# Kernel optimization log

Hardware: AMD Instinct MI355X
Metric: run time of the kernel (lower is better)

## Reference

```python
import jax, jax.numpy as jnp
import numpy as np

B, T, F = 64, 8192, 6
MODES, WIDTH, LAYERS = 32, 64, 4
FC1, OUT = 128, 7


def setup_inputs() -> dict:
    key = jax.random.key(0)
    ks = jax.random.split(key, 8)
    def glorot(k, shape, fan_in, fan_out):
        return jax.random.normal(k, shape, jnp.float32) * np.float32(np.sqrt(2.0 / (fan_in + fan_out)))
    inputs = jax.random.normal(ks[0], (B, T, F), jnp.float32)
    fc0_w = glorot(ks[1], (F, WIDTH), F, WIDTH)
    fc0_b = jnp.zeros((WIDTH,), jnp.float32)
    fourier_wr = glorot(ks[2], (LAYERS, MODES, WIDTH, WIDTH), WIDTH, WIDTH)
    fourier_wi = glorot(ks[3], (LAYERS, MODES, WIDTH, WIDTH), WIDTH, WIDTH)
    conv_w = glorot(ks[4], (LAYERS, WIDTH, WIDTH), WIDTH, WIDTH)
    conv_b = jnp.zeros((LAYERS, WIDTH), jnp.float32)
    fc1_w = glorot(ks[5], (WIDTH, FC1), WIDTH, FC1)
    fc1_b = jnp.zeros((FC1,), jnp.float32)
    fc2_w = glorot(ks[6], (FC1, OUT), FC1, OUT)
    fc2_b = jnp.zeros((OUT,), jnp.float32)
    return {"inputs": inputs, "fc0_w": fc0_w, "fc0_b": fc0_b,
            "fourier_wr": fourier_wr, "fourier_wi": fourier_wi,
            "conv_w": conv_w, "conv_b": conv_b,
            "fc1_w": fc1_w, "fc1_b": fc1_b, "fc2_w": fc2_w, "fc2_b": fc2_b}


def _fourier_layer_time(x, wr, wi):
    # x: [B, T, C]; wr/wi: [MODES, C, C]
    t = x.shape[1]
    x_ft = jnp.fft.rfft(x, axis=1)              # [B, T//2+1, C] complex64
    tfreq = x_ft.shape[1]
    m = min(MODES, tfreq)
    w = (wr[:m] + 1j * wi[:m]).astype(jnp.complex64)   # [m, C, C]
    out_ft = jnp.einsum('bmc,mco->bmo', x_ft[:, :m, :], w)  # [B, m, C]
    out_ft = jnp.pad(out_ft, ((0, 0), (0, tfreq - m), (0, 0)))  # zero high modes
    return jnp.fft.irfft(out_ft, n=t, axis=1)   # [B, T, C] float32


def reference(inputs, fc0_w, fc0_b, fourier_wr, fourier_wi, conv_w, conv_b,
              fc1_w, fc1_b, fc2_w, fc2_b):
    x = inputs @ fc0_w + fc0_b                  # [B, T, WIDTH]
    for i in range(LAYERS):
        xf = _fourier_layer_time(x, fourier_wr[i], fourier_wi[i])
        x = jax.nn.gelu(xf + x @ conv_w[i] + conv_b[i], approximate=False)
    x = jax.nn.gelu(x @ fc1_w + fc1_b, approximate=False)   # [B, T, 128]
    out = x @ fc2_w + fc2_b                     # [B, T, 7]
    out = out.reshape(B, T, OUT, 1)
    return out[:, -1, :, :]                     # [B, 7, 1]
```

## Files before the change

kernel.cpp:

```cpp
#include <hip/hip_runtime.h>
#include <math.h>


constexpr int B = 64, T = 8192, F = 6, MODES = 32, C = 64, FC1N = 128, OUTN = 7;
constexpr int TMASK = T - 1;
constexpr int GCHF = 8;
constexpr int GCHC = 4;
constexpr int OSTR = 68;

typedef __attribute__((ext_vector_type(4))) float f32x4;
typedef __attribute__((ext_vector_type(8))) short s16x8;
typedef const __attribute__((address_space(1))) unsigned* gas_ptr;
typedef __attribute__((address_space(3))) unsigned* las_ptr;

__device__ __forceinline__ float gelu_exact(float v) {
    return 0.5f * v * (1.0f + erff(v * 0.70710678118654752f));
}
__device__ __forceinline__ float gelu_fast(float v) {
    float z = fabsf(v) * 0.70710678118654752f;
    float t = __builtin_amdgcn_rcpf(fmaf(0.3275911f, z, 1.0f));
    float p = fmaf(t, 1.061405429f, -1.453152027f);
    p = fmaf(t, p, 1.421413741f);
    p = fmaf(t, p, -0.284496736f);
    p = fmaf(t, p, 0.254829592f);
    p = p * t;
    float e = __expf(-z * z);
    float erfv = copysignf(fmaf(-p, e, 1.0f), v);
    return 0.5f * v * (1.0f + erfv);
}
__device__ __forceinline__ unsigned short bf16_rne(float f) {
    unsigned u = __float_as_uint(f);
    unsigned r = u + 0x7FFFu + ((u >> 16) & 1u);
    return (unsigned short)(r >> 16);
}
__device__ __forceinline__ float bf16_f(unsigned short h) {
    return __uint_as_float(((unsigned)h) << 16);
}
__device__ __forceinline__ unsigned pack_split(float v) {
    unsigned short hi = bf16_rne(v);
    float lo = v - bf16_f(hi);
    return (((unsigned)hi) << 16) | (unsigned)bf16_rne(lo);
}
__device__ __forceinline__ s16x8 u4_to_s8(uint4 v) {
    union { uint4 u; s16x8 s; } cv; cv.u = v; return cv.s;
}
__device__ __forceinline__ s16x8 hi8(uint4 p0, uint4 p1) {
    uint4 h;
    h.x = __byte_perm(p0.x, p0.y, 0x7632); h.y = __byte_perm(p0.z, p0.w, 0x7632);
    h.z = __byte_perm(p1.x, p1.y, 0x7632); h.w = __byte_perm(p1.z, p1.w, 0x7632);
    return u4_to_s8(h);
}
__device__ __forceinline__ s16x8 lo8(uint4 p0, uint4 p1) {
    uint4 h;
    h.x = __byte_perm(p0.x, p0.y, 0x5410); h.y = __byte_perm(p0.z, p0.w, 0x5410);
    h.z = __byte_perm(p1.x, p1.y, 0x5410); h.w = __byte_perm(p1.z, p1.w, 0x5410);
    return u4_to_s8(h);
}

__global__ void twdtab_k(unsigned short* __restrict__ twdH, unsigned short* __restrict__ twdL) {
    int i = blockIdx.x * 256 + threadIdx.x;
    int t = i >> 6, j = i & 63, k = j & 31;
    int m = (k * t) & TMASK;
    double th = 6.283185307179586476925286766559 * (double)m / (double)T;
    float v = (float)((j < 32) ? cos(th) : sin(th));
    unsigned short hi = bf16_rne(v);
    twdH[i] = hi;
    twdL[i] = bf16_rne(v - bf16_f(hi));
}

__global__ void twdtabT_k(unsigned* __restrict__ twdTP) {
    int i = blockIdx.x * 256 + threadIdx.x;
    int j = i >> 13, t = i & TMASK, k = j & 31;
    int m = (k * t) & TMASK;
    double th = 6.283185307179586476925286766559 * (double)m / (double)T;
    float v = (float)((j < 32) ? cos(th) : sin(th));
    twdTP[i] = pack_split(v);
}

__global__ void __launch_bounds__(256) fc0dft_k(const float* __restrict__ in,
                                                const float* __restrict__ w,
                                                const float* __restrict__ bias,
                                                const unsigned* __restrict__ twdTP,
                                                unsigned* __restrict__ x,
                                                float* __restrict__ partF) {
    __shared__ unsigned outT[64 * OSTR];
    int b = blockIdx.y, tid = threadIdx.x;
    int wv = tid >> 6, lane = tid & 63;
    int l15 = lane & 15, quad = lane >> 4;
    size_t bT = (size_t)b * T;

    int rr = tid & 15, cg = (tid >> 4) * 4;
    float wl[F][4], bl[4];
#pragma unroll
    for (int f = 0; f < F; f++)
#pragma unroll
        for (int j = 0; j < 4; j++) wl[f][j] = w[f * C + cg + j];
#pragma unroll
    for (int j = 0; j < 4; j++) bl[j] = bias[cg + j];

    const unsigned* atp = twdTP + (size_t)(wv * 16 + l15) * T;
    f32x4 dftacc[4];
#pragma unroll
    for (int nt = 0; nt < 4; nt++) dftacc[nt] = (f32x4){0.f, 0.f, 0.f, 0.f};

    int t0 = blockIdx.x * (64 * GCHF);
    for (int g = 0; g < GCHF; g++) {
        int tb = t0 + g * 64;
#pragma unroll
        for (int i = 0; i < 4; i++) {
            int r = rr + i * 16;
            int trow = tb + r;
            const float* ip = in + ((size_t)b * T + trow) * F;
            float i0 = ip[0], i1 = ip[1], i2 = ip[2], i3 = ip[3], i4 = ip[4], i5 = ip[5];
            uint4 pk;
            unsigned pv[4];
#pragma unroll
            for (int j = 0; j < 4; j++) {
                float v = bl[j];
                v = fmaf(i0, wl[0][j], v); v = fmaf(i1, wl[1][j], v);
                v = fmaf(i2, wl[2][j], v); v = fmaf(i3, wl[3][j], v);
                v = fmaf(i4, wl[4][j], v); v = fmaf(i5, wl[5][j], v);
                pv[j] = pack_split(v);
            }
            pk.x = pv[0]; pk.y = pv[1]; pk.z = pv[2]; pk.w = pv[3];
            *(uint4*)(x + (bT + trow) * C + cg) = pk;
            outT[(cg + 0) * OSTR + r] = pv[0];
            outT[(cg + 1) * OSTR + r] = pv[1];
            outT[(cg + 2) * OSTR + r] = pv[2];
            outT[(cg + 3) * OSTR + r] = pv[3];
        }
        __syncthreads();
#pragma unroll
        for (int ks = 0; ks < 2; ks++) {
            const unsigned* ap = atp + tb + ks * 32 + quad * 8;
            uint4 a0 = *(const uint4*)ap;
            uint4 a1 = *(const uint4*)(ap + 4);
            s16x8 ah = hi8(a0, a1), al = lo8(a0, a1);
#pragma unroll
            for (int nt = 0; nt < 4; nt++) {
                const unsigned* bp = &outT[(nt * 16 + l15) * OSTR + ks * 32 + quad * 8];
                uint4 b0 = *(const uint4*)bp;
                uint4 b1 = *(const uint4*)(bp + 4);
                s16x8 bh = hi8(b0, b1), bl2 = lo8(b0, b1);
                dftacc[nt] = __builtin_amdgcn_mfma_f32_16x16x32_bf16(ah, bh, dftacc[nt], 0, 0, 0);
                dftacc[nt] = __builtin_amdgcn_mfma_f32_16x16x32_bf16(ah, bl2, dftacc[nt], 0, 0, 0);
                dftacc[nt] = __builtin_amdgcn_mfma_f32_16x16x32_bf16(al, bh, dftacc[nt], 0, 0, 0);
            }
        }
        __syncthreads();
    }
    float sgn = (wv >= 2) ? -1.f : 1.f;
#pragma unroll
    for (int nt = 0; nt < 4; nt++)
#pragma unroll
        for (int r = 0; r < 4; r++) {
            int j = wv * 16 + quad * 4 + r;
            unsafeAtomicAdd(&partF[((size_t)b * 64 + j) * 64 + nt * 16 + l15],
                            sgn * dftacc[nt][r]);
        }
}

__global__ void mode_mix(const float* __restrict__ partF, const float* __restrict__ wr,
                         const float* __restrict__ wi, float2* __restrict__ Y) {
    int b = blockIdx.y, k = blockIdx.x, o = threadIdx.x;
    __shared__ float xr[C], xi[C];
    xr[o] = partF[((size_t)b * 64 + k) * 64 + o];
    xi[o] = partF[((size_t)b * 64 + 32 + k) * 64 + o];
    __syncthreads();
    float ar = 0.f, ai = 0.f;
    for (int c = 0; c < C; c++) {
        float wrr = wr[((size_t)k * C + c) * C + o];
        float wii = wi[((size_t)k * C + c) * C + o];
        float Xr = xr[c], Xi = xi[c];
        ar = fmaf(Xr, wrr, ar); ar = fmaf(-Xi, wii, ar);
        ai = fmaf(Xr, wii, ai); ai = fmaf(Xi, wrr, ai);
    }
    Y[((size_t)b * MODES + k) * C + o] = make_float2(ar, ai);
}

__global__ void bweights_k(const float2* __restrict__ Y, const float* __restrict__ cw,
                           unsigned short* __restrict__ Bw) {
    int b = blockIdx.x, tid = threadIdx.x;
    const float invT = 1.0f / (float)T;
    for (int i = tid; i < C * 256; i += 256) {
        int o = i >> 8, kc = i & 255;
        int src = kc & 127, half = kc >> 7;
        float w;
        if (src < 32) {
            float s = (src == 0) ? invT : 2.0f * invT;
            w = s * Y[((size_t)b * MODES + src) * C + o].x;
        } else if (src < 64) {
            w = (-2.0f * invT) * Y[((size_t)b * MODES + (src - 32)) * C + o].y;
        } else {
            w = cw[(size_t)(src - 64) * C + o];
        }
        unsigned short hi = bf16_rne(w);
        Bw[((size_t)b * C + o) * 256 + kc] = half ? bf16_rne(w - bf16_f(hi)) : hi;
    }
}

__global__ void __launch_bounds__(256) combine_mfma(unsigned* __restrict__ xp,
                                                    const unsigned short* __restrict__ twdH,
                                                    const unsigned short* __restrict__ twdL,
                                                    const unsigned* __restrict__ twdTP,
                                                    const unsigned short* __restrict__ Bw,
                                                    const float* __restrict__ cb,
                                                    float* __restrict__ partF) {
    __shared__ unsigned xs[2][4096];
    int b = blockIdx.y;
    int tid = threadIdx.x;
    int wv = tid >> 6, lane = tid & 63;
    int lm = lane & 15, quad = lane >> 4;
    int ncol = wv * 16 + lm;
    size_t bT = (size_t)b * T;
    int sA = (lm & 7) * 4;

    const unsigned short* bwp = Bw + ((size_t)b * C + ncol) * 256 + quad * 8;
    s16x8 bf0 = *(const s16x8*)(bwp + 0);
    s16x8 bf1 = *(const s16x8*)(bwp + 32);
    s16x8 bf2 = *(const s16x8*)(bwp + 64);
    s16x8 bf3 = *(const s16x8*)(bwp + 96);
    s16x8 bf4 = *(const s16x8*)(bwp + 128);
    s16x8 bf5 = *(const s16x8*)(bwp + 160);
    s16x8 bf6 = *(const s16x8*)(bwp + 192);
    s16x8 bf7 = *(const s16x8*)(bwp + 224);
    float cbv = cb[ncol];

    const unsigned* atp = twdTP + (size_t)(wv * 16 + lm) * T;
    f32x4 dftacc[4];
#pragma unroll
    for (int nt = 0; nt < 4; nt++) dftacc[nt] = (f32x4){0.f, 0.f, 0.f, 0.f};

    int g0 = blockIdx.x * GCHC;
    const unsigned* cbase = xp + (bT + (size_t)g0 * 64) * C;

    int soff[4];
#pragma unroll
    for (int p = 0; p < 4; p++) {
        int L = tid * 4 + p * 1024;
        int r = L >> 6, cl = L & 63;
        soff[p] = r * 64 + (cl ^ ((r & 7) * 4));
    }
#pragma unroll
    for (int p = 0; p < 4; p++)
        __builtin_amdgcn_global_load_lds((gas_ptr)(cbase + soff[p]),
                                         (las_ptr)(&xs[0][tid * 4 + p * 1024]), 16, 0, 0);

    for (int g = 0; g < GCHC; g++) {
        int t0 = (g0 + g) * 64;
        asm volatile("s_waitcnt vmcnt(0)" ::: "memory");
        __syncthreads();
        if (g + 1 < GCHC) {
            const unsigned* nbase = cbase + (size_t)(g + 1) * 4096;
#pragma unroll
            for (int p = 0; p < 4; p++)
                __builtin_amdgcn_global_load_lds((gas_ptr)(nbase + soff[p]),
                                                 (las_ptr)(&xs[(g + 1) & 1][tid * 4 + p * 1024]),
                                                 16, 0, 0);
        }
        unsigned* buf = xs[g & 1];
        f32x4 acc[4];
#pragma unroll
        for (int mt = 0; mt < 4; mt++) acc[mt] = (f32x4){0.f, 0.f, 0.f, 0.f};

#pragma unroll
        for (int mt = 0; mt < 4; mt++) {
            int rr = mt * 16 + lm;
            int t = t0 + rr;
            const unsigned short* thp = twdH + (size_t)t * C + quad * 8;
            const unsigned short* tlp = twdL + (size_t)t * C + quad * 8;
            const unsigned* xrp = buf + rr * 64;
            int base0 = (quad * 8) ^ sA;
            s16x8 a;
            a = *(const s16x8*)thp;
            acc[mt] = __builtin_amdgcn_mfma_f32_16x16x32_bf16(a, bf0, acc[mt], 0, 0, 0);
            acc[mt] = __builtin_amdgcn_mfma_f32_16x16x32_bf16(a, bf4, acc[mt], 0, 0, 0);
            a = *(const s16x8*)(thp + 32);
            acc[mt] = __builtin_amdgcn_mfma_f32_16x16x32_bf16(a, bf1, acc[mt], 0, 0, 0);
            acc[mt] = __builtin_amdgcn_mfma_f32_16x16x32_bf16(a, bf5, acc[mt], 0, 0, 0);
            uint4 p0 = *(const uint4*)(xrp + base0);
            uint4 p1 = *(const uint4*)(xrp + (base0 ^ 4));
            a = hi8(p0, p1);
            acc[mt] = __builtin_amdgcn_mfma_f32_16x16x32_bf16(a, bf2, acc[mt], 0, 0, 0);
            acc[mt] = __builtin_amdgcn_mfma_f32_16x16x32_bf16(a, bf6, acc[mt], 0, 0, 0);
            uint4 p2 = *(const uint4*)(xrp + (base0 ^ 32));
            uint4 p3 = *(const uint4*)(xrp + (base0 ^ 36));
            a = hi8(p2, p3);
            acc[mt] = __builtin_amdgcn_mfma_f32_16x16x32_bf16(a, bf3, acc[mt], 0, 0, 0);
            acc[mt] = __builtin_amdgcn_mfma_f32_16x16x32_bf16(a, bf7, acc[mt], 0, 0, 0);
            a = *(const s16x8*)tlp;
            acc[mt] = __builtin_amdgcn_mfma_f32_16x16x32_bf16(a, bf0, acc[mt], 0, 0, 0);
            a = *(const s16x8*)(tlp + 32);
            acc[mt] = __builtin_amdgcn_mfma_f32_16x16x32_bf16(a, bf1, acc[mt], 0, 0, 0);
            a = lo8(p0, p1);
            acc[mt] = __builtin_amdgcn_mfma_f32_16x16x32_bf16(a, bf2, acc[mt], 0, 0, 0);
            a = lo8(p2, p3);
            acc[mt] = __builtin_amdgcn_mfma_f32_16x16x32_bf16(a, bf3, acc[mt], 0, 0, 0);
        }
        __syncthreads();
#pragma unroll
        for (int mt = 0; mt < 4; mt++) {
            uint4 pk;
            unsigned pv[4];
#pragma unroll
            for (int r = 0; r < 4; r++) {
                int t = t0 + mt * 16 + quad * 4 + r;
                float v = acc[mt][r] + cbv;
                pv[r] = pack_split(gelu_fast(v));
                xp[(bT + t) * C + ncol] = pv[r];
            }
            pk.x = pv[0]; pk.y = pv[1]; pk.z = pv[2]; pk.w = pv[3];
            *(uint4*)(&buf[ncol * 64 + ((mt * 16 + quad * 4) ^ sA)]) = pk;
        }
        __syncthreads();
#pragma unroll
        for (int ks = 0; ks < 2; ks++) {
            const unsigned* ap = atp + t0 + ks * 32 + quad * 8;
            uint4 a0 = *(const uint4*)ap;
            uint4 a1 = *(const uint4*)(ap + 4);
            s16x8 ah = hi8(a0, a1), al = lo8(a0, a1);
#pragma unroll
            for (int nt = 0; nt < 4; nt++) {
                int cd = nt * 16 + lm;
                const unsigned* bpb = buf + cd * 64;
                int tb0 = (ks * 32 + quad * 8) ^ sA;
                uint4 b0 = *(const uint4*)(bpb + tb0);
                uint4 b1 = *(const uint4*)(bpb + (tb0 ^ 4));
                s16x8 bh = hi8(b0, b1), bl2 = lo8(b0, b1);
                dftacc[nt] = __builtin_amdgcn_mfma_f32_16x16x32_bf16(ah, bh, dftacc[nt], 0, 0, 0);
                dftacc[nt] = __builtin_amdgcn_mfma_f32_16x16x32_bf16(ah, bl2, dftacc[nt], 0, 0, 0);
                dftacc[nt] = __builtin_amdgcn_mfma_f32_16x16x32_bf16(al, bh, dftacc[nt], 0, 0, 0);
            }
        }
    }
    float sgn = (wv >= 2) ? -1.f : 1.f;
#pragma unroll
    for (int nt = 0; nt < 4; nt++)
#pragma unroll
        for (int r = 0; r < 4; r++) {
            int j = wv * 16 + quad * 4 + r;
            unsafeAtomicAdd(&partF[((size_t)b * 64 + j) * 64 + nt * 16 + lm],
                            sgn * dftacc[nt][r]);
        }
}

__global__ void final_k(const unsigned* __restrict__ x3, const float2* __restrict__ Y3,
                        const float* __restrict__ cw, const float* __restrict__ cb,
                        const float* __restrict__ w1, const float* __restrict__ b1,
                        const float* __restrict__ w2, const float* __restrict__ b2,
                        float* __restrict__ out) {
    int b = blockIdx.x, tid = threadIdx.x;
    __shared__ float xrow[C];
    __shared__ float xl[C];
    __shared__ float h[FC1N];
    if (tid < C) {
        unsigned u = x3[((size_t)b * T + (T - 1)) * C + tid];
        xrow[tid] = __uint_as_float(u & 0xFFFF0000u) + __uint_as_float(u << 16);
    }
    __syncthreads();
    if (tid < C) {
        int o = tid;
        const float2* Yb = Y3 + (size_t)b * (MODES * C);
        float a2 = 0.f;
        for (int k = 1; k < MODES; k++) {
            float thk = 7.6699039394282067e-4f * (float)k;
            float cwv = cosf(thk), swv = -sinf(thk);
            float2 y = Yb[k * C + o];
            a2 = fmaf(y.x, cwv, a2);
            a2 = fmaf(-y.y, swv, a2);
        }
        float xf = (Yb[o].x + 2.f * a2) * (1.0f / (float)T);
        float cv = cb[o];
        for (int c = 0; c < C; c++) cv = fmaf(xrow[c], cw[c * C + o], cv);
        xl[o] = gelu_exact(xf + cv);
    }
    __syncthreads();
    {
        int j = tid;
        float acc = b1[j];
        for (int c = 0; c < C; c++) acc = fmaf(xl[c], w1[c * FC1N + j], acc);
        h[j] = gelu_exact(acc);
    }
    __syncthreads();
    if (tid < OUTN) {
        float acc = b2[tid];
        for (int j = 0; j < FC1N; j++) acc = fmaf(h[j], w2[j * OUTN + tid], acc);
        out[b * OUTN + tid] = acc;
    }
}

extern "C" void kernel_launch(void* const* d_in, const int* in_sizes, int n_in,
                              void* d_out, int out_size, void* d_ws, size_t ws_size,
                              hipStream_t stream) {
    const float* inp   = (const float*)d_in[0];
    const float* fc0_w = (const float*)d_in[1];
    const float* fc0_b = (const float*)d_in[2];
    const float* fwr   = (const float*)d_in[3];
    const float* fwi   = (const float*)d_in[4];
    const float* cw    = (const float*)d_in[5];
    const float* cb    = (const float*)d_in[6];
    const float* w1    = (const float*)d_in[7];
    const float* b1    = (const float*)d_in[8];
    const float* w2    = (const float*)d_in[9];
    const float* b2    = (const float*)d_in[10];
    float* out = (float*)d_out;

    char* ws = (char*)d_ws;
    unsigned* x = (unsigned*)ws;
    size_t off = (size_t)B * T * C * sizeof(unsigned);
    float* partF = (float*)(ws + off);
    const size_t PART_BYTES = (size_t)B * 64 * 64 * sizeof(float);
    off += PART_BYTES;
    float2* Y = (float2*)(ws + off);
    off += (size_t)B * MODES * C * sizeof(float2);
    unsigned short* twdH = (unsigned short*)(ws + off);
    off += (size_t)T * C * sizeof(unsigned short);
    unsigned short* twdL = (unsigned short*)(ws + off);
    off += (size_t)T * C * sizeof(unsigned short);
    unsigned* twdTP = (unsigned*)(ws + off);
    off += (size_t)64 * T * sizeof(unsigned);
    unsigned short* Bw = (unsigned short*)(ws + off);
    off += (size_t)B * C * 256 * sizeof(unsigned short);

    twdtab_k<<<(T * C) / 256, 256, 0, stream>>>(twdH, twdL);
    twdtabT_k<<<(64 * T) / 256, 256, 0, stream>>>(twdTP);

    hipMemsetAsync(partF, 0, PART_BYTES, stream);
    fc0dft_k<<<dim3(T / (64 * GCHF), B), 256, 0, stream>>>(inp, fc0_w, fc0_b, twdTP, x, partF);

    for (int l = 0; l < 4; l++) {
        mode_mix<<<dim3(MODES, B), 64, 0, stream>>>(partF, fwr + (size_t)l * MODES * C * C,
                                                    fwi + (size_t)l * MODES * C * C, Y);
        if (l < 3) {
            hipMemsetAsync(partF, 0, PART_BYTES, stream);
            bweights_k<<<B, 256, 0, stream>>>(Y, cw + (size_t)l * C * C, Bw);
            combine_mfma<<<dim3(T / (64 * GCHC), B), 256, 0, stream>>>(x, twdH, twdL, twdTP, Bw,
                                                                       cb + (size_t)l * C, partF);
        }
    }
    final_k<<<B, FC1N, 0, stream>>>(x, Y, cw + (size_t)3 * C * C, cb + (size_t)3 * C,
                                    w1, b1, w2, b2, out);
}
```

Baseline: 553.8 us.

## Split twiddle tables into hi/lo planes, fuse mode-mix with weight build, retime prefetch

The transposed twiddle table is stored as separate bf16 hi and lo arrays, so the DFT A-fragments can be loaded directly instead of being unpacked with byte permutes. These loads are hoisted to the start of each chunk, and the fc0 input rows are read as float2 vectors. The mode_mix and bweights kernels are fused into one kernel with 256-thread blocks, removing a launch and a round trip of Y through memory. In combine_mfma, __syncthreads is replaced with hand-written waitcnt/barrier asm and the next-chunk LDS prefetch is issued later, after the first compute phase. The hand-tuned vmcnt count is a correctness risk if the compiler schedules loads differently than assumed.

After: 525.9 us. -5.0%, faster.

```diff
diff --git a/kernel.cpp b/kernel.cpp
--- a/kernel.cpp
+++ b/kernel.cpp
@@ -68,19 +68,22 @@
     twdL[i] = bf16_rne(v - bf16_f(hi));
 }
 
-__global__ void twdtabT_k(unsigned* __restrict__ twdTP) {
+__global__ void twdtabT_k(unsigned short* __restrict__ twdTPH, unsigned short* __restrict__ twdTPL) {
     int i = blockIdx.x * 256 + threadIdx.x;
     int j = i >> 13, t = i & TMASK, k = j & 31;
     int m = (k * t) & TMASK;
     double th = 6.283185307179586476925286766559 * (double)m / (double)T;
     float v = (float)((j < 32) ? cos(th) : sin(th));
-    twdTP[i] = pack_split(v);
+    unsigned short hi = bf16_rne(v);
+    twdTPH[i] = hi;
+    twdTPL[i] = bf16_rne(v - bf16_f(hi));
 }
 
 __global__ void __launch_bounds__(256) fc0dft_k(const float* __restrict__ in,
                                                 const float* __restrict__ w,
                                                 const float* __restrict__ bias,
-                                                const unsigned* __restrict__ twdTP,
+                                                const unsigned short* __restrict__ twdTPH,
+                                                const unsigned short* __restrict__ twdTPL,
                                                 unsigned* __restrict__ x,
                                                 float* __restrict__ partF) {
     __shared__ unsigned outT[64 * OSTR];
@@ -98,7 +101,8 @@
 #pragma unroll
     for (int j = 0; j < 4; j++) bl[j] = bias[cg + j];
 
-    const unsigned* atp = twdTP + (size_t)(wv * 16 + l15) * T;
+    const unsigned short* atpH = twdTPH + (size_t)(wv * 16 + l15) * T;
+    const unsigned short* atpL = twdTPL + (size_t)(wv * 16 + l15) * T;
     f32x4 dftacc[4];
 #pragma unroll
     for (int nt = 0; nt < 4; nt++) dftacc[nt] = (f32x4){0.f, 0.f, 0.f, 0.f};
@@ -106,12 +110,22 @@
     int t0 = blockIdx.x * (64 * GCHF);
     for (int g = 0; g < GCHF; g++) {
         int tb = t0 + g * 64;
+        float2 rin[4][3];
+#pragma unroll
+        for (int i = 0; i < 4; i++) {
+            const float2* ip2 = (const float2*)(in + ((size_t)b * T + tb + rr + i * 16) * F);
+            rin[i][0] = ip2[0]; rin[i][1] = ip2[1]; rin[i][2] = ip2[2];
+        }
+        s16x8 dAh0 = *(const s16x8*)(atpH + tb + quad * 8);
+        s16x8 dAl0 = *(const s16x8*)(atpL + tb + quad * 8);
+        s16x8 dAh1 = *(const s16x8*)(atpH + tb + 32 + quad * 8);
+        s16x8 dAl1 = *(const s16x8*)(atpL + tb + 32 + quad * 8);
 #pragma unroll
         for (int i = 0; i < 4; i++) {
             int r = rr + i * 16;
             int trow = tb + r;
-            const float* ip = in + ((size_t)b * T + trow) * F;
-            float i0 = ip[0], i1 = ip[1], i2 = ip[2], i3 = ip[3], i4 = ip[4], i5 = ip[5];
+            float i0 = rin[i][0].x, i1 = rin[i][0].y, i2 = rin[i][1].x;
+            float i3 = rin[i][1].y, i4 = rin[i][2].x, i5 = rin[i][2].y;
             uint4 pk;
             unsigned pv[4];
 #pragma unroll
@@ -129,13 +143,11 @@
             outT[(cg + 2) * OSTR + r] = pv[2];
             outT[(cg + 3) * OSTR + r] = pv[3];
         }
-        __syncthreads();
+        asm volatile("s_waitcnt lgkmcnt(0)\n\ts_barrier" ::: "memory");
 #pragma unroll
         for (int ks = 0; ks < 2; ks++) {
-            const unsigned* ap = atp + tb + ks * 32 + quad * 8;
-            uint4 a0 = *(const uint4*)ap;
-            uint4 a1 = *(const uint4*)(ap + 4);
-            s16x8 ah = hi8(a0, a1), al = lo8(a0, a1);
+            s16x8 ah = ks ? dAh1 : dAh0;
+            s16x8 al = ks ? dAl1 : dAl0;
 #pragma unroll
             for (int nt = 0; nt < 4; nt++) {
                 const unsigned* bp = &outT[(nt * 16 + l15) * OSTR + ks * 32 + quad * 8];
@@ -147,7 +159,7 @@
                 dftacc[nt] = __builtin_amdgcn_mfma_f32_16x16x32_bf16(al, bh, dftacc[nt], 0, 0, 0);
             }
         }
-        __syncthreads();
+        asm volatile("s_waitcnt lgkmcnt(0)\n\ts_barrier" ::: "memory");
     }
     float sgn = (wv >= 2) ? -1.f : 1.f;
 #pragma unroll
@@ -160,49 +172,64 @@
         }
 }
 
-__global__ void mode_mix(const float* __restrict__ partF, const float* __restrict__ wr,
-                         const float* __restrict__ wi, float2* __restrict__ Y) {
-    int b = blockIdx.y, k = blockIdx.x, o = threadIdx.x;
-    __shared__ float xr[C], xi[C];
-    xr[o] = partF[((size_t)b * 64 + k) * 64 + o];
-    xi[o] = partF[((size_t)b * 64 + 32 + k) * 64 + o];
+__global__ void __launch_bounds__(256) mixbw_k(const float* __restrict__ partF,
+                                               const float* __restrict__ wr,
+                                               const float* __restrict__ wi,
+                                               const float* __restrict__ cw,
+                                               float2* __restrict__ Y,
+                                               unsigned short* __restrict__ Bw,
+                                               int writeBw) {
+    __shared__ float xr[32][64], xi[32][64];
+    int b = blockIdx.x, q = blockIdx.y, tid = threadIdx.x;
+    int o = tid & 63, ks = tid >> 6;
+    const float* pb = partF + (size_t)b * 4096;
+    for (int i = tid; i < 2048; i += 256) xr[i >> 6][i & 63] = pb[i];
+    for (int i = tid; i < 2048; i += 256) xi[i >> 6][i & 63] = pb[2048 + i];
     __syncthreads();
-    float ar = 0.f, ai = 0.f;
-    for (int c = 0; c < C; c++) {
-        float wrr = wr[((size_t)k * C + c) * C + o];
-        float wii = wi[((size_t)k * C + c) * C + o];
-        float Xr = xr[c], Xi = xi[c];
-        ar = fmaf(Xr, wrr, ar); ar = fmaf(-Xi, wii, ar);
-        ai = fmaf(Xr, wii, ai); ai = fmaf(Xi, wrr, ai);
-    }
-    Y[((size_t)b * MODES + k) * C + o] = make_float2(ar, ai);
-}
-
-__global__ void bweights_k(const float2* __restrict__ Y, const float* __restrict__ cw,
-                           unsigned short* __restrict__ Bw) {
-    int b = blockIdx.x, tid = threadIdx.x;
     const float invT = 1.0f / (float)T;
-    for (int i = tid; i < C * 256; i += 256) {
-        int o = i >> 8, kc = i & 255;
-        int src = kc & 127, half = kc >> 7;
-        float w;
-        if (src < 32) {
-            float s = (src == 0) ? invT : 2.0f * invT;
-            w = s * Y[((size_t)b * MODES + src) * C + o].x;
-        } else if (src < 64) {
-            w = (-2.0f * invT) * Y[((size_t)b * MODES + (src - 32)) * C + o].y;
-        } else {
-            w = cw[(size_t)(src - 64) * C + o];
-        }
-        unsigned short hi = bf16_rne(w);
-        Bw[((size_t)b * C + o) * 256 + kc] = half ? bf16_rne(w - bf16_f(hi)) : hi;
+#pragma unroll
+    for (int s = 0; s < 2; s++) {
+        int k = q * 8 + ks * 2 + s;
+        float ar = 0.f, ai = 0.f;
+        const float* wrk = wr + (size_t)k * 4096 + o;
+        const float* wik = wi + (size_t)k * 4096 + o;
+        for (int c = 0; c < 64; c++) {
+            float wrr = wrk[(size_t)c * 64];
+            float wii = wik[(size_t)c * 64];
+            float Xr = xr[k][c], Xi = xi[k][c];
+            ar = fmaf(Xr, wrr, ar); ar = fmaf(-Xi, wii, ar);
+            ai = fmaf(Xr, wii, ai); ai = fmaf(Xi, wrr, ai);
+        }
+        Y[((size_t)b * MODES + k) * C + o] = make_float2(ar, ai);
+        if (writeBw) {
+            size_t base = ((size_t)b * C + o) * 256;
+            float s0 = (k == 0) ? invT : 2.0f * invT;
+            float w0 = s0 * ar;
+            unsigned short h0 = bf16_rne(w0);
+            Bw[base + k] = h0;
+            Bw[base + 128 + k] = bf16_rne(w0 - bf16_f(h0));
+            float w1 = (-2.0f * invT) * ai;
+            unsigned short h1 = bf16_rne(w1);
+            Bw[base + 32 + k] = h1;
+            Bw[base + 160 + k] = bf16_rne(w1 - bf16_f(h1));
+        }
+    }
+    if (writeBw && q == 0) {
+        for (int i = tid; i < 4096; i += 256) {
+            int c = i >> 6, oo = i & 63;
+            float w = cw[(size_t)c * C + oo];
+            unsigned short h = bf16_rne(w);
+            Bw[((size_t)b * C + oo) * 256 + 64 + c] = h;
+            Bw[((size_t)b * C + oo) * 256 + 192 + c] = bf16_rne(w - bf16_f(h));
+        }
     }
 }
 
 __global__ void __launch_bounds__(256) combine_mfma(unsigned* __restrict__ xp,
                                                     const unsigned short* __restrict__ twdH,
                                                     const unsigned short* __restrict__ twdL,
-                                                    const unsigned* __restrict__ twdTP,
+                                                    const unsigned short* __restrict__ twdTPH,
+                                                    const unsigned short* __restrict__ twdTPL,
                                                     const unsigned short* __restrict__ Bw,
                                                     const float* __restrict__ cb,
                                                     float* __restrict__ partF) {
@@ -226,7 +253,8 @@
     s16x8 bf7 = *(const s16x8*)(bwp + 224);
     float cbv = cb[ncol];
 
-    const unsigned* atp = twdTP + (size_t)(wv * 16 + lm) * T;
+    const unsigned short* atpH = twdTPH + (size_t)(wv * 16 + lm) * T;
+    const unsigned short* atpL = twdTPL + (size_t)(wv * 16 + lm) * T;
     f32x4 dftacc[4];
 #pragma unroll
     for (int nt = 0; nt < 4; nt++) dftacc[nt] = (f32x4){0.f, 0.f, 0.f, 0.f};
@@ -246,18 +274,17 @@
         __builtin_amdgcn_global_load_lds((gas_ptr)(cbase + soff[p]),
                                          (las_ptr)(&xs[0][tid * 4 + p * 1024]), 16, 0, 0);
 
+#pragma unroll
     for (int g = 0; g < GCHC; g++) {
         int t0 = (g0 + g) * 64;
-        asm volatile("s_waitcnt vmcnt(0)" ::: "memory");
-        __syncthreads();
-        if (g + 1 < GCHC) {
-            const unsigned* nbase = cbase + (size_t)(g + 1) * 4096;
-#pragma unroll
-            for (int p = 0; p < 4; p++)
-                __builtin_amdgcn_global_load_lds((gas_ptr)(nbase + soff[p]),
-                                                 (las_ptr)(&xs[(g + 1) & 1][tid * 4 + p * 1024]),
-                                                 16, 0, 0);
-        }
+        if (g == 0) asm volatile("s_waitcnt vmcnt(0)\n\ts_barrier" ::: "memory");
+        else        asm volatile("s_waitcnt vmcnt(16)\n\ts_barrier" ::: "memory");
+
+        s16x8 dAh0 = *(const s16x8*)(atpH + t0 + quad * 8);
+        s16x8 dAl0 = *(const s16x8*)(atpL + t0 + quad * 8);
+        s16x8 dAh1 = *(const s16x8*)(atpH + t0 + 32 + quad * 8);
+        s16x8 dAl1 = *(const s16x8*)(atpL + t0 + 32 + quad * 8);
+
         unsigned* buf = xs[g & 1];
         f32x4 acc[4];
 #pragma unroll
@@ -297,7 +324,16 @@
             a = lo8(p2, p3);
             acc[mt] = __builtin_amdgcn_mfma_f32_16x16x32_bf16(a, bf3, acc[mt], 0, 0, 0);
         }
-        __syncthreads();
+        asm volatile("s_waitcnt lgkmcnt(0)\n\ts_barrier" ::: "memory");
+
+        if (g + 1 < GCHC) {
+            const unsigned* nbase = cbase + (size_t)(g + 1) * 4096;
+#pragma unroll
+            for (int p = 0; p < 4; p++)
+                __builtin_amdgcn_global_load_lds((gas_ptr)(nbase + soff[p]),
+                                                 (las_ptr)(&xs[(g + 1) & 1][tid * 4 + p * 1024]),
+                                                 16, 0, 0);
+        }
 #pragma unroll
         for (int mt = 0; mt < 4; mt++) {
             uint4 pk;
@@ -312,13 +348,12 @@
             pk.x = pv[0]; pk.y = pv[1]; pk.z = pv[2]; pk.w = pv[3];
             *(uint4*)(&buf[ncol * 64 + ((mt * 16 + quad * 4) ^ sA)]) = pk;
         }
-        __syncthreads();
+        asm volatile("s_waitcnt lgkmcnt(0)\n\ts_barrier" ::: "memory");
+
 #pragma unroll
         for (int ks = 0; ks < 2; ks++) {
-            const unsigned* ap = atp + t0 + ks * 32 + quad * 8;
-            uint4 a0 = *(const uint4*)ap;
-            uint4 a1 = *(const uint4*)(ap + 4);
-            s16x8 ah = hi8(a0, a1), al = lo8(a0, a1);
+            s16x8 ah = ks ? dAh1 : dAh0;
+            s16x8 al = ks ? dAl1 : dAl0;
 #pragma unroll
             for (int nt = 0; nt < 4; nt++) {
                 int cd = nt * 16 + lm;
@@ -417,24 +452,29 @@
     off += (size_t)T * C * sizeof(unsigned short);
     unsigned short* twdL = (unsigned short*)(ws + off);
     off += (size_t)T * C * sizeof(unsigned short);
-    unsigned* twdTP = (unsigned*)(ws + off);
-    off += (size_t)64 * T * sizeof(unsigned);
+    unsigned short* twdTPH = (unsigned short*)(ws + off);
+    off += (size_t)64 * T * sizeof(unsigned short);
+    unsigned short* twdTPL = (unsigned short*)(ws + off);
+    off += (size_t)64 * T * sizeof(unsigned short);
     unsigned short* Bw = (unsigned short*)(ws + off);
     off += (size_t)B * C * 256 * sizeof(unsigned short);
 
     twdtab_k<<<(T * C) / 256, 256, 0, stream>>>(twdH, twdL);
-    twdtabT_k<<<(64 * T) / 256, 256, 0, stream>>>(twdTP);
+    twdtabT_k<<<(64 * T) / 256, 256, 0, stream>>>(twdTPH, twdTPL);
 
     hipMemsetAsync(partF, 0, PART_BYTES, stream);
-    fc0dft_k<<<dim3(T / (64 * GCHF), B), 256, 0, stream>>>(inp, fc0_w, fc0_b, twdTP, x, partF);
+    fc0dft_k<<<dim3(T / (64 * GCHF), B), 256, 0, stream>>>(inp, fc0_w, fc0_b,
+                                                           twdTPH, twdTPL, x, partF);
 
     for (int l = 0; l < 4; l++) {
-        mode_mix<<<dim3(MODES, B), 64, 0, stream>>>(partF, fwr + (size_t)l * MODES * C * C,
-                                                    fwi + (size_t)l * MODES * C * C, Y);
+        mixbw_k<<<dim3(B, 4), 256, 0, stream>>>(partF, fwr + (size_t)l * MODES * C * C,
+                                                fwi + (size_t)l * MODES * C * C,
+                                                cw + (size_t)l * C * C, Y, Bw,
+                                                (l < 3) ? 1 : 0);
         if (l < 3) {
             hipMemsetAsync(partF, 0, PART_BYTES, stream);
-            bweights_k<<<B, 256, 0, stream>>>(Y, cw + (size_t)l * C * C, Bw);
-            combine_mfma<<<dim3(T / (64 * GCHC), B), 256, 0, stream>>>(x, twdH, twdL, twdTP, Bw,
+            combine_mfma<<<dim3(T / (64 * GCHC), B), 256, 0, stream>>>(x, twdH, twdL,
+                                                                       twdTPH, twdTPL, Bw,
                                                                        cb + (size_t)l * C, partF);
         }
     }
```
